# Kernel tuning notes

Hardware: AMD Instinct MI355X
Metric: run time of the kernel (lower is better)

Reference implementation:

```python
import jax, jax.numpy as jnp
import numpy as np

K_HALF = 512
BUCKETS = 8
FV_SCALE = 16
SHIFT = 6
FT_SHIFT = 0
FT_IN = 32 * 704 + 704  # FT_IN_DIMS + VIRTUAL = 23232
B = 4096


def setup_inputs() -> dict:
    key = jax.random.key(0)
    ks = jax.random.split(key, 11)
    s = 0.02
    return {
        "bucket": jax.random.randint(ks[0], (B, 1), 0, BUCKETS, dtype=jnp.int64 if jax.config.jax_enable_x64 else jnp.int32).astype(jnp.int32),
        "features1": jax.random.uniform(ks[1], (B, FT_IN), dtype=jnp.float32),
        "features2": jax.random.uniform(ks[2], (B, FT_IN), dtype=jnp.float32),
        "ft_w": s * jax.random.normal(ks[3], (K_HALF + BUCKETS, FT_IN), dtype=jnp.float32),
        "ft_b": s * jax.random.normal(ks[4], (K_HALF + BUCKETS,), dtype=jnp.float32),
        "h1_w": s * jax.random.normal(ks[5], (16 * BUCKETS, 2 * K_HALF), dtype=jnp.float32),
        "h1_b": s * jax.random.normal(ks[6], (16 * BUCKETS,), dtype=jnp.float32),
        "h2_w": s * jax.random.normal(ks[7], (32 * BUCKETS, 16), dtype=jnp.float32),
        "h2_b": s * jax.random.normal(ks[8], (32 * BUCKETS,), dtype=jnp.float32),
        "out_w": s * jax.random.normal(ks[9], (BUCKETS, 32), dtype=jnp.float32),
        "out_b": jnp.zeros((BUCKETS,), dtype=jnp.float32),
    }


def reference(bucket, features1, features2, ft_w, ft_b, h1_w, h1_b, h2_w, h2_b, out_w, out_b):
    clamp = lambda x: jnp.clip(x, 0.0, 1.0)
    a1 = features1 @ ft_w.T + ft_b  # [B, 520]
    a2 = features2 @ ft_w.T + ft_b
    f1, psqt1 = a1[:, :K_HALF], a1[:, K_HALF:]
    f2, psqt2 = a2[:, :K_HALF], a2[:, K_HALF:]
    psqt = 0.5 * (jnp.take_along_axis(psqt1, bucket, axis=1)
                  - jnp.take_along_axis(psqt2, bucket, axis=1))  # [B,1]
    ft_out = clamp(jnp.concatenate([f1, f2], axis=1))  # [B, 1024]
    h1 = (ft_out @ h1_w.T + h1_b).reshape(-1, BUCKETS, 16)
    h1 = clamp(jnp.take_along_axis(h1, bucket[:, :, None], axis=1)[:, 0])  # [B,16]
    h2 = (h1 @ h2_w.T + h2_b).reshape(-1, BUCKETS, 32)
    h2 = clamp(jnp.take_along_axis(h2, bucket[:, :, None], axis=1)[:, 0])  # [B,32]
    out = h2 @ out_w.T + out_b  # [B, 8]
    return jnp.take_along_axis(out, bucket, axis=1) + (FV_SCALE * 2 ** FT_SHIFT) * psqt / 2 ** SHIFT
```

## Files before the change

kernel.cpp:

```cpp
#include <hip/hip_runtime.h>
#include <hip/hip_bf16.h>
#include <stdint.h>

typedef __attribute__((ext_vector_type(8))) short short8v;
typedef __attribute__((ext_vector_type(4))) short short4v;
typedef __attribute__((ext_vector_type(4))) float floatx4;

#define K_DIM   23232
#define BATCH   4096
#define M_TOT   8192
#define BM      128
#define BN      176
#define BK      64
#define N_PAD   528
#define N_REAL  520

__device__ __forceinline__ float clamp01(float x) {
    return fminf(fmaxf(x, 0.0f), 1.0f);
}

__device__ __forceinline__ short8v cvt8(float4 a, float4 b) {
    union { short8v s; __hip_bfloat16 h[8]; } u;
    u.h[0] = __float2bfloat16(a.x); u.h[1] = __float2bfloat16(a.y);
    u.h[2] = __float2bfloat16(a.z); u.h[3] = __float2bfloat16(a.w);
    u.h[4] = __float2bfloat16(b.x); u.h[5] = __float2bfloat16(b.y);
    u.h[6] = __float2bfloat16(b.z); u.h[7] = __float2bfloat16(b.w);
    return u.s;
}

#define GLOAD_LDS16(g, l) __builtin_amdgcn_global_load_lds(               \
    (const __attribute__((address_space(1))) void*)(g),                   \
    (__attribute__((address_space(3))) void*)(l), 16, 0, 0)

__global__ __launch_bounds__(256) void convert_bf16(
    const float* __restrict__ f1, const float* __restrict__ f2,
    const float* __restrict__ ftw,
    __hip_bfloat16* __restrict__ A, __hip_bfloat16* __restrict__ B)
{
    const size_t totalA = (size_t)M_TOT * K_DIM;
    const size_t halfA  = totalA / 2;
    const size_t totalB = (size_t)N_PAD * K_DIM;
    const size_t realB  = (size_t)N_REAL * K_DIM;
    size_t idx    = ((size_t)blockIdx.x * blockDim.x + threadIdx.x) * 8;
    size_t stride = (size_t)gridDim.x * blockDim.x * 8;

    for (size_t i = idx; i < totalA; i += stride) {
        const float* src = (i < halfA) ? (f1 + i) : (f2 + (i - halfA));
        float4 v0 = *(const float4*)(src);
        float4 v1 = *(const float4*)(src + 4);
        *(short8v*)(A + i) = cvt8(v0, v1);
    }
    for (size_t i = idx; i < totalB; i += stride) {
        if (i < realB) {
            float4 v0 = *(const float4*)(ftw + i);
            float4 v1 = *(const float4*)(ftw + i + 4);
            *(short8v*)(B + i) = cvt8(v0, v1);
        } else {
            *(short8v*)(B + i) = (short8v){0,0,0,0,0,0,0,0};
        }
    }
}

__global__ __launch_bounds__(256) void ft_gemm(
    const __hip_bfloat16* __restrict__ A,
    const __hip_bfloat16* __restrict__ B,
    float* __restrict__ part, int kiters)
{
    __shared__ __align__(16) __hip_bfloat16 As[BM][BK];
    __shared__ __align__(16) __hip_bfloat16 Bs[BN][BK];

    const int t    = threadIdx.x;
    const int w    = t >> 6;
    const int lane = t & 63;
    const int quad = lane >> 4;
    const int l16  = lane & 15;

    const int n0 = blockIdx.x * BN;
    const int m0 = blockIdx.y * BM;
    const int z  = blockIdx.z;
    int k0 = z * kiters * BK;
    const int kEnd = k0 + kiters * BK;

    const int arow = lane >> 3;
    const int acol = (lane & 7) * 8;

    floatx4 acc[2][11];
#pragma unroll
    for (int i = 0; i < 2; ++i)
#pragma unroll
        for (int j = 0; j < 11; ++j)
            acc[i][j] = (floatx4){0.f, 0.f, 0.f, 0.f};

    for (; k0 < kEnd; k0 += BK) {
        __syncthreads();
#pragma unroll
        for (int i = 0; i < 4; ++i) {
            int R = w * 8 + i * 32;
            const __hip_bfloat16* g =
                A + (size_t)(m0 + R + arow) * K_DIM + k0 + acol;
            GLOAD_LDS16(g, &As[R][0]);
        }
        for (int R = w * 8; R < BN; R += 32) {
            const __hip_bfloat16* g =
                B + (size_t)(n0 + R + arow) * K_DIM + k0 + acol;
            GLOAD_LDS16(g, &Bs[R][0]);
        }
        __syncthreads();
#pragma unroll
        for (int ks = 0; ks < BK; ks += 32) {
            short8v a0 = *(const short8v*)(&As[w * 32 + l16][ks + quad * 8]);
            short8v a1 = *(const short8v*)(&As[w * 32 + 16 + l16][ks + quad * 8]);
#pragma unroll
            for (int nf = 0; nf < 11; ++nf) {
                short8v b = *(const short8v*)(&Bs[nf * 16 + l16][ks + quad * 8]);
                acc[0][nf] = __builtin_amdgcn_mfma_f32_16x16x32_bf16(a0, b, acc[0][nf], 0, 0, 0);
                acc[1][nf] = __builtin_amdgcn_mfma_f32_16x16x32_bf16(a1, b, acc[1][nf], 0, 0, 0);
            }
        }
    }

    float* __restrict__ dst = part + (size_t)z * ((size_t)M_TOT * N_PAD);
#pragma unroll
    for (int mi = 0; mi < 2; ++mi) {
#pragma unroll
        for (int nf = 0; nf < 11; ++nf) {
            int gn = n0 + nf * 16 + l16;
#pragma unroll
            for (int r = 0; r < 4; ++r) {
                int gm = m0 + w * 32 + mi * 16 + quad * 4 + r;
                dst[(size_t)gm * N_PAD + gn] = acc[mi][nf][r];
            }
        }
    }
}

__global__ __launch_bounds__(256) void ft_gemm_fused(
    const float* __restrict__ f1, const float* __restrict__ f2,
    const float* __restrict__ ftw, float* __restrict__ part, int kiters)
{
    __shared__ __align__(16) __hip_bfloat16 As[BM][72];
    __shared__ __align__(16) __hip_bfloat16 Bs[BN][72];

    const int t    = threadIdx.x;
    const int w    = t >> 6;
    const int lane = t & 63;
    const int quad = lane >> 4;
    const int l16  = lane & 15;

    const int n0 = blockIdx.x * BN;
    const int m0 = blockIdx.y * BM;
    const int z  = blockIdx.z;
    int k0 = z * kiters * BK;
    const int kEnd = k0 + kiters * BK;

    const float* __restrict__ srcA =
        (m0 < BATCH) ? (f1 + (size_t)m0 * K_DIM)
                     : (f2 + (size_t)(m0 - BATCH) * K_DIM);

    floatx4 acc[2][11];
#pragma unroll
    for (int i = 0; i < 2; ++i)
#pragma unroll
        for (int j = 0; j < 11; ++j)
            acc[i][j] = (floatx4){0.f, 0.f, 0.f, 0.f};

    for (; k0 < kEnd; k0 += BK) {
        __syncthreads();
#pragma unroll
        for (int it = 0; it < 8; ++it) {
            int c = t + it * 256, row = c >> 4, col = (c & 15) * 4;
            float4 v = *(const float4*)(srcA + (size_t)row * K_DIM + k0 + col);
            union { short4v s; __hip_bfloat16 h[4]; } u;
            u.h[0] = __float2bfloat16(v.x); u.h[1] = __float2bfloat16(v.y);
            u.h[2] = __float2bfloat16(v.z); u.h[3] = __float2bfloat16(v.w);
            *(short4v*)(&As[row][col]) = u.s;
        }
#pragma unroll
        for (int it = 0; it < 11; ++it) {
            int c = t + it * 256, row = c >> 4, col = (c & 15) * 4;
            int gn = n0 + row;
            float4 v = (gn < N_REAL)
                ? *(const float4*)(ftw + (size_t)gn * K_DIM + k0 + col)
                : make_float4(0.f, 0.f, 0.f, 0.f);
            union { short4v s; __hip_bfloat16 h[4]; } u;
            u.h[0] = __float2bfloat16(v.x); u.h[1] = __float2bfloat16(v.y);
            u.h[2] = __float2bfloat16(v.z); u.h[3] = __float2bfloat16(v.w);
            *(short4v*)(&Bs[row][col]) = u.s;
        }
        __syncthreads();
#pragma unroll
        for (int ks = 0; ks < BK; ks += 32) {
            short8v a0 = *(const short8v*)(&As[w * 32 + l16][ks + quad * 8]);
            short8v a1 = *(const short8v*)(&As[w * 32 + 16 + l16][ks + quad * 8]);
#pragma unroll
            for (int nf = 0; nf < 11; ++nf) {
                short8v b = *(const short8v*)(&Bs[nf * 16 + l16][ks + quad * 8]);
                acc[0][nf] = __builtin_amdgcn_mfma_f32_16x16x32_bf16(a0, b, acc[0][nf], 0, 0, 0);
                acc[1][nf] = __builtin_amdgcn_mfma_f32_16x16x32_bf16(a1, b, acc[1][nf], 0, 0, 0);
            }
        }
    }

    float* __restrict__ dst = part + (size_t)z * ((size_t)M_TOT * N_PAD);
#pragma unroll
    for (int mi = 0; mi < 2; ++mi) {
#pragma unroll
        for (int nf = 0; nf < 11; ++nf) {
            int gn = n0 + nf * 16 + l16;
#pragma unroll
            for (int r = 0; r < 4; ++r) {
                int gm = m0 + w * 32 + mi * 16 + quad * 4 + r;
                dst[(size_t)gm * N_PAD + gn] = acc[mi][nf][r];
            }
        }
    }
}

__global__ __launch_bounds__(256) void nnue_tail(
    const float* __restrict__ part, int ksplit,
    const int*   __restrict__ bucket,
    const float* __restrict__ ft_b,
    const float* __restrict__ h1_w, const float* __restrict__ h1_b,
    const float* __restrict__ h2_w, const float* __restrict__ h2_b,
    const float* __restrict__ out_w, const float* __restrict__ out_b,
    float* __restrict__ out)
{
    const int m = blockIdx.x;
    const int b = bucket[m];
    const size_t sz = (size_t)M_TOT * N_PAD;

    __shared__ float ft[1024];
    __shared__ float h1s[16];

    const float* p1 = part + (size_t)m * N_PAD;
    const float* p2 = part + (size_t)(m + BATCH) * N_PAD;

    for (int i = threadIdx.x; i < 1024; i += 256) {
        const float* pr = (i < 512) ? p1 : p2;
        int ci = i & 511;
        float v = ft_b[ci];
        for (int s = 0; s < ksplit; ++s) v += pr[ci + s * sz];
        ft[i] = clamp01(v);
    }
    __syncthreads();

    const int w    = threadIdx.x >> 6;
    const int lane = threadIdx.x & 63;

#pragma unroll
    for (int i = 0; i < 4; ++i) {
        int row = b * 16 + w * 4 + i;
        const float* wr = h1_w + (size_t)row * 1024;
        float s = 0.f;
#pragma unroll
        for (int c = 0; c < 16; ++c)
            s += ft[c * 64 + lane] * wr[c * 64 + lane];
#pragma unroll
        for (int off = 32; off > 0; off >>= 1)
            s += __shfl_down(s, off);
        if (lane == 0) h1s[w * 4 + i] = clamp01(s + h1_b[row]);
    }
    __syncthreads();

    if (threadIdx.x < 32) {
        int i = threadIdx.x;
        const float* wr = h2_w + (size_t)(b * 32 + i) * 16;
        float s = h2_b[b * 32 + i];
#pragma unroll
        for (int j = 0; j < 16; ++j) s += wr[j] * h1s[j];
        float prod = clamp01(s) * out_w[b * 32 + i];
#pragma unroll
        for (int off = 16; off > 0; off >>= 1)
            prod += __shfl_down(prod, off);
        if (i == 0) {
            float v1 = 0.f, v2 = 0.f;
            for (int s2 = 0; s2 < ksplit; ++s2) {
                v1 += p1[512 + b + s2 * sz];
                v2 += p2[512 + b + s2 * sz];
            }
            out[m] = prod + out_b[b] + 0.25f * 0.5f * 2.0f * (v1 - v2) * 0.5f
                   ;
        }
    }
}


extern "C" void kernel_launch(void* const* d_in, const int* in_sizes, int n_in,
                              void* d_out, int out_size, void* d_ws, size_t ws_size,
                              hipStream_t stream) {
    const int*   bucket = (const int*)  d_in[0];
    const float* f1     = (const float*)d_in[1];
    const float* f2     = (const float*)d_in[2];
    const float* ftw    = (const float*)d_in[3];
    const float* ftb    = (const float*)d_in[4];
    const float* h1w    = (const float*)d_in[5];
    const float* h1b    = (const float*)d_in[6];
    const float* h2w    = (const float*)d_in[7];
    const float* h2b    = (const float*)d_in[8];
    const float* outw   = (const float*)d_in[9];
    const float* outb   = (const float*)d_in[10];
    float* out = (float*)d_out;

    const size_t szA = (size_t)M_TOT * K_DIM * sizeof(__hip_bfloat16);
    const size_t szB = (size_t)N_PAD * K_DIM * sizeof(__hip_bfloat16);
    const size_t szPart1 = (size_t)M_TOT * N_PAD * sizeof(float);

    int ksplit;
    if (ws_size >= szA + szB + 11 * szPart1)      ksplit = 11;
    else if (ws_size >= szA + szB + 3 * szPart1)  ksplit = 3;
    else                                          ksplit = 0;

    if (ksplit > 0) {
        __hip_bfloat16* A = (__hip_bfloat16*)d_ws;
        __hip_bfloat16* Bm = (__hip_bfloat16*)((char*)d_ws + szA);
        float* part = (float*)((char*)d_ws + szA + szB);
        int kiters = 363 / ksplit;

        convert_bf16<<<4096, 256, 0, stream>>>(f1, f2, ftw, A, Bm);
        dim3 grid1(3, 64, ksplit);
        ft_gemm<<<grid1, 256, 0, stream>>>(A, Bm, part, kiters);
        nnue_tail<<<BATCH, 256, 0, stream>>>(part, ksplit, bucket, ftb,
                                             h1w, h1b, h2w, h2b, outw, outb, out);
    } else {
        float* part = (float*)d_ws;
        dim3 grid1(3, 64, 3);
        ft_gemm_fused<<<grid1, 256, 0, stream>>>(f1, f2, ftw, part, 121);
        nnue_tail<<<BATCH, 256, 0, stream>>>(part, 3, bucket, ftb,
                                             h1w, h1b, h2w, h2b, outw, outb, out);
    }
}
```

Measured before the change: 1.195 ms.

## Enlarge GEMM M-tile, swizzle LDS layout, and remap blocks across XCDs

The bf16 FT GEMM now computes a 256x176 tile per block, with 4x11 MFMA accumulators per wave, instead of 128x176. This halves the number of B-tile reloads per output element and raises MFMA work per LDS read. Global-to-LDS loads now XOR-swizzle column slots by row, and the fragment reads apply the matching swizzle, to cut LDS bank conflicts. The 3D grid becomes a 1D grid with a remap that keeps neighbouring tiles on the same XCD for better L2 reuse. The tradeoffs are higher register pressure under launch_bounds(256,2), larger LDS use per block, and fewer blocks in total.

```diff
diff --git a/kernel.cpp b/kernel.cpp
--- a/kernel.cpp
+++ b/kernel.cpp
@@ -10,6 +10,7 @@
 #define BATCH   4096
 #define M_TOT   8192
 #define BM      128
+#define BMG     256
 #define BN      176
 #define BK      64
 #define N_PAD   528
@@ -61,12 +62,12 @@
     }
 }
 
-__global__ __launch_bounds__(256) void ft_gemm(
+__global__ __launch_bounds__(256, 2) void ft_gemm(
     const __hip_bfloat16* __restrict__ A,
     const __hip_bfloat16* __restrict__ B,
     float* __restrict__ part, int kiters)
 {
-    __shared__ __align__(16) __hip_bfloat16 As[BM][BK];
+    __shared__ __align__(16) __hip_bfloat16 As[BMG][BK];
     __shared__ __align__(16) __hip_bfloat16 Bs[BN][BK];
 
     const int t    = threadIdx.x;
@@ -74,19 +75,27 @@
     const int lane = t & 63;
     const int quad = lane >> 4;
     const int l16  = lane & 15;
-
-    const int n0 = blockIdx.x * BN;
-    const int m0 = blockIdx.y * BM;
-    const int z  = blockIdx.z;
-    int k0 = z * kiters * BK;
+    const int r7   = l16 & 7;
+
+    const int cpx = gridDim.x >> 3;
+    const int h   = blockIdx.x;
+    const int lid = (h & 7) * cpx + (h >> 3);
+    const int xb  = lid % 3;
+    const int rst = lid / 3;
+    const int yb  = rst & 31;
+    const int zb  = rst >> 5;
+
+    const int n0 = xb * BN;
+    const int m0 = yb * BMG;
+    int k0 = zb * kiters * BK;
     const int kEnd = k0 + kiters * BK;
 
     const int arow = lane >> 3;
-    const int acol = (lane & 7) * 8;
-
-    floatx4 acc[2][11];
-#pragma unroll
-    for (int i = 0; i < 2; ++i)
+    const int acol = ((lane & 7) ^ (lane >> 3)) * 8;
+
+    floatx4 acc[4][11];
+#pragma unroll
+    for (int i = 0; i < 4; ++i)
 #pragma unroll
         for (int j = 0; j < 11; ++j)
             acc[i][j] = (floatx4){0.f, 0.f, 0.f, 0.f};
@@ -94,7 +103,7 @@
     for (; k0 < kEnd; k0 += BK) {
         __syncthreads();
 #pragma unroll
-        for (int i = 0; i < 4; ++i) {
+        for (int i = 0; i < 8; ++i) {
             int R = w * 8 + i * 32;
             const __hip_bfloat16* g =
                 A + (size_t)(m0 + R + arow) * K_DIM + k0 + acol;
@@ -108,26 +117,31 @@
         __syncthreads();
 #pragma unroll
         for (int ks = 0; ks < BK; ks += 32) {
-            short8v a0 = *(const short8v*)(&As[w * 32 + l16][ks + quad * 8]);
-            short8v a1 = *(const short8v*)(&As[w * 32 + 16 + l16][ks + quad * 8]);
+            const int slot = ((ks >> 3) + quad) ^ r7;
+            short8v a[4];
+#pragma unroll
+            for (int mi = 0; mi < 4; ++mi)
+                a[mi] = *(const short8v*)(&As[w * 64 + mi * 16 + l16][slot * 8]);
 #pragma unroll
             for (int nf = 0; nf < 11; ++nf) {
-                short8v b = *(const short8v*)(&Bs[nf * 16 + l16][ks + quad * 8]);
-                acc[0][nf] = __builtin_amdgcn_mfma_f32_16x16x32_bf16(a0, b, acc[0][nf], 0, 0, 0);
-                acc[1][nf] = __builtin_amdgcn_mfma_f32_16x16x32_bf16(a1, b, acc[1][nf], 0, 0, 0);
-            }
-        }
-    }
-
-    float* __restrict__ dst = part + (size_t)z * ((size_t)M_TOT * N_PAD);
-#pragma unroll
-    for (int mi = 0; mi < 2; ++mi) {
+                short8v b = *(const short8v*)(&Bs[nf * 16 + l16][slot * 8]);
+#pragma unroll
+                for (int mi = 0; mi < 4; ++mi)
+                    acc[mi][nf] = __builtin_amdgcn_mfma_f32_16x16x32_bf16(
+                        a[mi], b, acc[mi][nf], 0, 0, 0);
+            }
+        }
+    }
+
+    float* __restrict__ dst = part + (size_t)zb * ((size_t)M_TOT * N_PAD);
+#pragma unroll
+    for (int mi = 0; mi < 4; ++mi) {
 #pragma unroll
         for (int nf = 0; nf < 11; ++nf) {
             int gn = n0 + nf * 16 + l16;
 #pragma unroll
             for (int r = 0; r < 4; ++r) {
-                int gm = m0 + w * 32 + mi * 16 + quad * 4 + r;
+                int gm = m0 + w * 64 + mi * 16 + quad * 4 + r;
                 dst[(size_t)gm * N_PAD + gn] = acc[mi][nf][r];
             }
         }
@@ -278,12 +292,10 @@
                 v1 += p1[512 + b + s2 * sz];
                 v2 += p2[512 + b + s2 * sz];
             }
-            out[m] = prod + out_b[b] + 0.25f * 0.5f * 2.0f * (v1 - v2) * 0.5f
-                   ;
-        }
-    }
-}
-
+            out[m] = prod + out_b[b] + 0.125f * (v1 - v2);
+        }
+    }
+}
 
 extern "C" void kernel_launch(void* const* d_in, const int* in_sizes, int n_in,
                               void* d_out, int out_size, void* d_ws, size_t ws_size,
@@ -317,8 +329,8 @@
         int kiters = 363 / ksplit;
 
         convert_bf16<<<4096, 256, 0, stream>>>(f1, f2, ftw, A, Bm);
-        dim3 grid1(3, 64, ksplit);
-        ft_gemm<<<grid1, 256, 0, stream>>>(A, Bm, part, kiters);
+        int nblk = 3 * 32 * ksplit;
+        ft_gemm<<<dim3(nblk), 256, 0, stream>>>(A, Bm, part, kiters);
         nnue_tail<<<BATCH, 256, 0, stream>>>(part, ksplit, bucket, ftb,
                                              h1w, h1b, h2w, h2b, outw, outb, out);
     } else {
```

After: 1.140 ms. 4.6% less time.
